# Kernel tuning notes

Measured on AMD Instinct MI355X. Metric: run time of the kernel, lower is better.

Reference implementation:

```python
import jax, jax.numpy as jnp
import numpy as np

BG_ID = 0
RADIUS = 10
MODE = 'gauss'
LAMBDA_B = 1.0
GAMMA = 0.1
TEMP = 4.0
EPS = 1e-8
BIG = 1e6  # stands in for +inf (no fg in a row/column); BIG**2 is fp32-safe


def setup_inputs() -> dict:
    key = jax.random.key(0)
    k1, k2 = jax.random.split(key)
    B, C, H, W = 4, 19, 256, 256
    return {
        'student_logits': jax.random.normal(k1, (B, C, H, W), jnp.float32),
        'teacher_logits': jax.random.normal(k2, (B, C, H, W), jnp.float32),
    }


def _edt2(fg):
    """Exact squared Euclidean distance transform of (1 - fg):
    distance from each pixel to the nearest foreground pixel.
    Separable algorithm: 1D column pass (two cumulative scans), then
    exact lower-envelope minimization along rows (vectorized brute force).
    fg: bool [B, H, W]. Returns float32 [B, H, W]."""
    B, H, W = fg.shape
    ii = jnp.arange(H, dtype=jnp.float32)[None, :, None]  # row index
    # 1D vertical distance to nearest fg pixel in each column
    d_fwd = ii - jax.lax.cummax(jnp.where(fg, ii, -BIG), axis=1)
    d_bwd = -jax.lax.cummax(jnp.where(fg, -ii, -BIG), axis=1, reverse=True) - ii
    g = jnp.minimum(jnp.minimum(d_fwd, d_bwd), BIG)  # [B,H,W]
    # exact 2D squared EDT: dist2[b,i,j] = min_{j'} (j-j')^2 + g[b,i,j']^2
    jj = jnp.arange(W, dtype=jnp.float32)
    diff2 = (jj[:, None] - jj[None, :]) ** 2  # [W, W']
    dist2 = jnp.min(diff2[None, None, :, :] + (g * g)[:, :, None, :], axis=-1)
    return dist2


def _erode(fg):
    """scipy.ndimage.binary_erosion with 4-connected cross structure and
    border_value=0 (out-of-bounds treated as background)."""
    p = jnp.pad(fg, ((0, 0), (1, 1), (1, 1)))
    return fg & p[:, :-2, 1:-1] & p[:, 2:, 1:-1] & p[:, 1:-1, :-2] & p[:, 1:-1, 2:]


def _weight_map(teacher_logits):
    # argmax of softmax(probs) == argmax of logits (softmax is monotone per-pixel)
    pred = jnp.argmax(teacher_logits, axis=1)  # [B,H,W]
    fg = pred != BG_ID
    dist2 = _edt2(fg)
    dist = jnp.sqrt(dist2)
    mask = (dist <= RADIUS).astype(jnp.float32)
    sigma = RADIUS / 2.0
    if MODE == 'gauss':
        wdist = jnp.exp(-dist2 / (2.0 * sigma * sigma))
    else:
        wdist = jnp.clip(1.0 - dist / RADIUS, 0.0, 1.0)
    wdist = wdist * mask
    boundary = (fg & ~_erode(fg)).astype(jnp.float32)
    # wb = wdist*(1+lambda_b*boundary); final weights = wb*mask_inside
    # (if an image has no fg pixels, dist is huge -> mask==0 -> weights==0,
    #  matching the scipy loop's `continue` which leaves zeros)
    return wdist * (1.0 + LAMBDA_B * boundary) * mask


def reference(student_logits, teacher_logits):
    weight_map = _weight_map(teacher_logits)  # [B,H,W]
    # teacher probs at temperature T (torch computes t_prob_T and t_prob
    # identically twice; computed once here)
    t_prob = jax.nn.softmax(teacher_logits / TEMP, axis=1)
    entropy = -jnp.sum(t_prob * jnp.log(jnp.clip(t_prob, EPS, None)), axis=1)
    ent_max = jnp.max(entropy, axis=(1, 2), keepdims=True)
    conf_factor = GAMMA + (1.0 - GAMMA) * (1.0 - entropy / (ent_max + EPS))
    s_logp = jax.nn.log_softmax(student_logits / TEMP, axis=1)
    kl_per_pixel = jnp.sum(t_prob * (jnp.log(t_prob + EPS) - s_logp), axis=1)
    total_weight = weight_map * conf_factor
    loss = jnp.sum(total_weight * kl_per_pixel) / (jnp.sum(total_weight) + EPS)
    return TEMP * TEMP * loss
```

## Files before the change

### kernel.cpp

```cpp
#include <hip/hip_runtime.h>
#include <math.h>

#define NC   19
#define HH   256
#define WW   256
#define NB   4
#define HW   (HH * WW)
#define NPIX (NB * HW)
#define CAP2 121.0f

__global__ __launch_bounds__(256) void k_pixel(
    const float* __restrict__ student, const float* __restrict__ teacher,
    float* __restrict__ entropy, float* __restrict__ kl,
    unsigned char* __restrict__ fg, float* __restrict__ bmax)
{
    const int p = blockIdx.x * 256 + threadIdx.x;
    const int b = p >> 16;
    const int r = p & (HW - 1);
    const float* tb = teacher + (size_t)b * NC * HW + r;
    const float* sb = student + (size_t)b * NC * HW + r;

    float St = 0.f, T1 = 0.f, T2 = 0.f, Ss = 0.f;
    float tmx = -INFINITY;
    int ax = 0;
#pragma unroll
    for (int c = 0; c < NC; ++c) {
        float tv = tb[(size_t)c * HW];
        float sv = sb[(size_t)c * HW];
        if (tv > tmx) { tmx = tv; ax = c; }
        float e = __expf(tv * 0.25f);
        St += e;
        T1 += e * tv;
        T2 += e * sv;
        Ss += __expf(sv * 0.25f);
    }
    float rSt = 1.0f / St;
    float ent = __logf(St) - 0.25f * T1 * rSt;
    float klv = __logf(Ss) - 0.25f * T2 * rSt - ent;

    entropy[p] = ent;
    kl[p]      = klv;
    fg[p]      = (ax != 0) ? 1 : 0;

    float m = ent;
#pragma unroll
    for (int o = 32; o >= 1; o >>= 1) m = fmaxf(m, __shfl_down(m, o, 64));
    __shared__ float red[4];
    int wave = threadIdx.x >> 6, lane = threadIdx.x & 63;
    if (lane == 0) red[wave] = m;
    __syncthreads();
    if (threadIdx.x == 0)
        bmax[blockIdx.x] = fmaxf(fmaxf(red[0], red[1]), fmaxf(red[2], red[3]));
}

#define TS   32
#define HALO 10
#define FW   (TS + 2 * HALO)

__global__ __launch_bounds__(256) void k_tile(
    const unsigned char* __restrict__ fg, const float* __restrict__ entropy,
    const float* __restrict__ kl, const float* __restrict__ bmax,
    double* __restrict__ part)
{
    __shared__ float  fgt[FW][FW];
    __shared__ float  vm[TS][FW];
    __shared__ float  red[4];
    __shared__ double snum[4], sden[4];

    const int b   = blockIdx.z;
    const int ti0 = blockIdx.y * TS;
    const int tj0 = blockIdx.x * TS;
    const int tid = threadIdx.x;
    const int wave = tid >> 6, lane = tid & 63;
    const unsigned char* fgb = fg + (size_t)b * HW;

    float m = bmax[(b << 8) + tid];
#pragma unroll
    for (int o = 32; o >= 1; o >>= 1) m = fmaxf(m, __shfl_down(m, o, 64));
    if (lane == 0) red[wave] = m;

    for (int l = tid; l < FW * FW; l += 256) {
        int li = l / FW, lj = l - li * FW;
        int gi = ti0 - HALO + li, gj = tj0 - HALO + lj;
        float v = 0.f;
        if (gi >= 0 && gi < HH && gj >= 0 && gj < WW) v = (float)fgb[gi * WW + gj];
        fgt[li][lj] = v;
    }
    __syncthreads();
    float em = fmaxf(fmaxf(red[0], red[1]), fmaxf(red[2], red[3]));

    for (int l = tid; l < TS * FW; l += 256) {
        int i = l / FW, jj = l - i * FW;
        float mn = CAP2;
#pragma unroll
        for (int di = -HALO; di <= HALO; ++di) {
            float fv = fgt[HALO + i + di][jj];
            mn = fminf(mn, (float)(di * di) + (1.0f - fv) * 1000.0f);
        }
        vm[i][jj] = mn;
    }
    __syncthreads();

    double num = 0.0, den = 0.0;
#pragma unroll
    for (int k = 0; k < (TS * TS) / 256; ++k) {
        int p = tid + k * 256;
        int i = p >> 5, j = p & (TS - 1);
        float d2 = CAP2;
#pragma unroll
        for (int dj = -HALO; dj <= HALO; ++dj)
            d2 = fminf(d2, (float)(dj * dj) + vm[i][j + HALO + dj]);
        float mask  = (d2 <= 100.0f) ? 1.0f : 0.0f;
        float wdist = __expf(-d2 * 0.02f) * mask;

        float f  = fgt[HALO + i][HALO + j];
        float up = fgt[HALO + i - 1][HALO + j];
        float dn = fgt[HALO + i + 1][HALO + j];
        float lf = fgt[HALO + i][HALO + j - 1];
        float rt = fgt[HALO + i][HALO + j + 1];
        float mn4 = fminf(fminf(up, dn), fminf(lf, rt));
        float boundary = (f != 0.f && mn4 == 0.f) ? 1.0f : 0.0f;

        float w = wdist * (1.0f + boundary) * mask;
        size_t gidx = (size_t)b * HW + (size_t)(ti0 + i) * WW + (tj0 + j);
        float conf = 0.1f + 0.9f * (1.0f - entropy[gidx] / (em + 1e-8f));
        float tw = w * conf;
        num += (double)(tw * kl[gidx]);
        den += (double)tw;
    }

#pragma unroll
    for (int o = 32; o >= 1; o >>= 1) {
        num += __shfl_down(num, o, 64);
        den += __shfl_down(den, o, 64);
    }
    if (lane == 0) { snum[wave] = num; sden[wave] = den; }
    __syncthreads();
    if (tid == 0) {
        int bid = (blockIdx.z << 6) + (blockIdx.y << 3) + blockIdx.x;
        part[bid * 2 + 0] = snum[0] + snum[1] + snum[2] + snum[3];
        part[bid * 2 + 1] = sden[0] + sden[1] + sden[2] + sden[3];
    }
}

__global__ __launch_bounds__(256) void k_final(
    const double* __restrict__ part, float* __restrict__ out)
{
    const int tid = threadIdx.x;
    double num = part[tid * 2 + 0];
    double den = part[tid * 2 + 1];
#pragma unroll
    for (int o = 32; o >= 1; o >>= 1) {
        num += __shfl_down(num, o, 64);
        den += __shfl_down(den, o, 64);
    }
    __shared__ double snum[4], sden[4];
    int wave = tid >> 6, lane = tid & 63;
    if (lane == 0) { snum[wave] = num; sden[wave] = den; }
    __syncthreads();
    if (tid == 0) {
        num = snum[0] + snum[1] + snum[2] + snum[3];
        den = sden[0] + sden[1] + sden[2] + sden[3];
        out[0] = (float)(16.0 * num / (den + 1e-8));
    }
}

extern "C" void kernel_launch(void* const* d_in, const int* in_sizes, int n_in,
                              void* d_out, int out_size, void* d_ws, size_t ws_size,
                              hipStream_t stream)
{
    const float* student = (const float*)d_in[0];
    const float* teacher = (const float*)d_in[1];
    float* out = (float*)d_out;

    char* ws = (char*)d_ws;
    double*        part    = (double*)(ws + 0);
    float*         bmax    = (float*)(ws + 8192);
    float*         entropy = (float*)(ws + 16384);
    float*         kl      = (float*)(ws + 16384 + (size_t)NPIX * 4);
    unsigned char* fg      = (unsigned char*)(ws + 16384 + (size_t)NPIX * 8);

    k_pixel<<<NPIX / 256, 256, 0, stream>>>(student, teacher, entropy, kl, fg, bmax);
    dim3 g2(WW / TS, HH / TS, NB);
    k_tile<<<g2, 256, 0, stream>>>(fg, entropy, kl, bmax, part);
    k_final<<<1, 256, 0, stream>>>(part, out);
}
```

Measured before the change: 87.37 us.

## Vectorize pixel pass and defer confidence normalization to final reduction

The per-pixel kernel now handles two adjacent pixels per thread with float2 loads and writes entropy and KL interleaved as one float2 array. The tile kernel no longer needs the global entropy maximum. It accumulates four weighted sums (w, w*ent, w*kl, w*ent*kl) so the confidence factor, which is linear in entropy, can be applied per batch in the final kernel. This removes the bmax reduction and the second load stream from the tile kernel. The cost is more double-precision accumulators and shuffles, a larger partials buffer, and half as many threads in the pixel kernel.

```diff
diff --git a/kernel.cpp b/kernel.cpp
--- a/kernel.cpp
+++ b/kernel.cpp
@@ -11,38 +11,43 @@
 
 __global__ __launch_bounds__(256) void k_pixel(
     const float* __restrict__ student, const float* __restrict__ teacher,
-    float* __restrict__ entropy, float* __restrict__ kl,
-    unsigned char* __restrict__ fg, float* __restrict__ bmax)
-{
-    const int p = blockIdx.x * 256 + threadIdx.x;
-    const int b = p >> 16;
-    const int r = p & (HW - 1);
+    float2* __restrict__ ekl, unsigned char* __restrict__ fg,
+    float* __restrict__ bmax)
+{
+    const int q = (blockIdx.x * 256 + threadIdx.x) * 2;
+    const int b = q >> 16;
+    const int r = q & (HW - 1);
     const float* tb = teacher + (size_t)b * NC * HW + r;
     const float* sb = student + (size_t)b * NC * HW + r;
 
-    float St = 0.f, T1 = 0.f, T2 = 0.f, Ss = 0.f;
-    float tmx = -INFINITY;
-    int ax = 0;
+    float Stx = 0.f, T1x = 0.f, T2x = 0.f, Ssx = 0.f;
+    float Sty = 0.f, T1y = 0.f, T2y = 0.f, Ssy = 0.f;
+    float tmx = -INFINITY, tmy = -INFINITY;
+    int ax = 0, ay = 0;
 #pragma unroll
     for (int c = 0; c < NC; ++c) {
-        float tv = tb[(size_t)c * HW];
-        float sv = sb[(size_t)c * HW];
-        if (tv > tmx) { tmx = tv; ax = c; }
-        float e = __expf(tv * 0.25f);
-        St += e;
-        T1 += e * tv;
-        T2 += e * sv;
-        Ss += __expf(sv * 0.25f);
-    }
-    float rSt = 1.0f / St;
-    float ent = __logf(St) - 0.25f * T1 * rSt;
-    float klv = __logf(Ss) - 0.25f * T2 * rSt - ent;
-
-    entropy[p] = ent;
-    kl[p]      = klv;
-    fg[p]      = (ax != 0) ? 1 : 0;
-
-    float m = ent;
+        float2 t2 = *(const float2*)(tb + (size_t)c * HW);
+        float2 s2 = *(const float2*)(sb + (size_t)c * HW);
+        if (t2.x > tmx) { tmx = t2.x; ax = c; }
+        if (t2.y > tmy) { tmy = t2.y; ay = c; }
+        float exx = __expf(t2.x * 0.25f);
+        float exy = __expf(t2.y * 0.25f);
+        Stx += exx;           Sty += exy;
+        T1x += exx * t2.x;    T1y += exy * t2.y;
+        T2x += exx * s2.x;    T2y += exy * s2.y;
+        Ssx += __expf(s2.x * 0.25f);
+        Ssy += __expf(s2.y * 0.25f);
+    }
+    float rStx = 1.0f / Stx, rSty = 1.0f / Sty;
+    float entx = __logf(Stx) - 0.25f * T1x * rStx;
+    float enty = __logf(Sty) - 0.25f * T1y * rSty;
+    float klx  = __logf(Ssx) - 0.25f * T2x * rStx - entx;
+    float kly  = __logf(Ssy) - 0.25f * T2y * rSty - enty;
+
+    *(float4*)(ekl + q) = make_float4(entx, klx, enty, kly);
+    *(uchar2*)(fg + q)  = make_uchar2(ax != 0, ay != 0);
+
+    float m = fmaxf(entx, enty);
 #pragma unroll
     for (int o = 32; o >= 1; o >>= 1) m = fmaxf(m, __shfl_down(m, o, 64));
     __shared__ float red[4];
@@ -58,14 +63,12 @@
 #define FW   (TS + 2 * HALO)
 
 __global__ __launch_bounds__(256) void k_tile(
-    const unsigned char* __restrict__ fg, const float* __restrict__ entropy,
-    const float* __restrict__ kl, const float* __restrict__ bmax,
+    const unsigned char* __restrict__ fg, const float2* __restrict__ ekl,
     double* __restrict__ part)
 {
     __shared__ float  fgt[FW][FW];
     __shared__ float  vm[TS][FW];
-    __shared__ float  red[4];
-    __shared__ double snum[4], sden[4];
+    __shared__ double sred[4][4];
 
     const int b   = blockIdx.z;
     const int ti0 = blockIdx.y * TS;
@@ -74,11 +77,6 @@
     const int wave = tid >> 6, lane = tid & 63;
     const unsigned char* fgb = fg + (size_t)b * HW;
 
-    float m = bmax[(b << 8) + tid];
-#pragma unroll
-    for (int o = 32; o >= 1; o >>= 1) m = fmaxf(m, __shfl_down(m, o, 64));
-    if (lane == 0) red[wave] = m;
-
     for (int l = tid; l < FW * FW; l += 256) {
         int li = l / FW, lj = l - li * FW;
         int gi = ti0 - HALO + li, gj = tj0 - HALO + lj;
@@ -87,7 +85,6 @@
         fgt[li][lj] = v;
     }
     __syncthreads();
-    float em = fmaxf(fmaxf(red[0], red[1]), fmaxf(red[2], red[3]));
 
     for (int l = tid; l < TS * FW; l += 256) {
         int i = l / FW, jj = l - i * FW;
@@ -101,7 +98,7 @@
     }
     __syncthreads();
 
-    double num = 0.0, den = 0.0;
+    double s0 = 0.0, s1 = 0.0, s2 = 0.0, s3 = 0.0;
 #pragma unroll
     for (int k = 0; k < (TS * TS) / 256; ++k) {
         int p = tid + k * 256;
@@ -122,45 +119,64 @@
         float boundary = (f != 0.f && mn4 == 0.f) ? 1.0f : 0.0f;
 
         float w = wdist * (1.0f + boundary) * mask;
-        size_t gidx = (size_t)b * HW + (size_t)(ti0 + i) * WW + (tj0 + j);
-        float conf = 0.1f + 0.9f * (1.0f - entropy[gidx] / (em + 1e-8f));
-        float tw = w * conf;
-        num += (double)(tw * kl[gidx]);
-        den += (double)tw;
+        float2 ek = ekl[(size_t)b * HW + (size_t)(ti0 + i) * WW + (tj0 + j)];
+        float we = w * ek.x;
+        s0 += (double)w;
+        s1 += (double)we;
+        s2 += (double)(w * ek.y);
+        s3 += (double)(we * ek.y);
     }
 
 #pragma unroll
     for (int o = 32; o >= 1; o >>= 1) {
-        num += __shfl_down(num, o, 64);
-        den += __shfl_down(den, o, 64);
-    }
-    if (lane == 0) { snum[wave] = num; sden[wave] = den; }
+        s0 += __shfl_down(s0, o, 64);
+        s1 += __shfl_down(s1, o, 64);
+        s2 += __shfl_down(s2, o, 64);
+        s3 += __shfl_down(s3, o, 64);
+    }
+    if (lane == 0) {
+        sred[wave][0] = s0; sred[wave][1] = s1;
+        sred[wave][2] = s2; sred[wave][3] = s3;
+    }
     __syncthreads();
     if (tid == 0) {
         int bid = (blockIdx.z << 6) + (blockIdx.y << 3) + blockIdx.x;
-        part[bid * 2 + 0] = snum[0] + snum[1] + snum[2] + snum[3];
-        part[bid * 2 + 1] = sden[0] + sden[1] + sden[2] + sden[3];
+        double* o = part + bid * 4;
+        o[0] = sred[0][0] + sred[1][0] + sred[2][0] + sred[3][0];
+        o[1] = sred[0][1] + sred[1][1] + sred[2][1] + sred[3][1];
+        o[2] = sred[0][2] + sred[1][2] + sred[2][2] + sred[3][2];
+        o[3] = sred[0][3] + sred[1][3] + sred[2][3] + sred[3][3];
     }
 }
 
 __global__ __launch_bounds__(256) void k_final(
-    const double* __restrict__ part, float* __restrict__ out)
+    const double* __restrict__ part, const float* __restrict__ bmax,
+    float* __restrict__ out)
 {
     const int tid = threadIdx.x;
-    double num = part[tid * 2 + 0];
-    double den = part[tid * 2 + 1];
+    const int b = tid >> 6, lane = tid & 63;
+
+    const double* ps = part + (size_t)(b * 64 + lane) * 4;
+    double s0 = ps[0], s1 = ps[1], s2 = ps[2], s3 = ps[3];
+    float em = fmaxf(bmax[b * 128 + lane], bmax[b * 128 + 64 + lane]);
 #pragma unroll
     for (int o = 32; o >= 1; o >>= 1) {
-        num += __shfl_down(num, o, 64);
-        den += __shfl_down(den, o, 64);
-    }
-    __shared__ double snum[4], sden[4];
-    int wave = tid >> 6, lane = tid & 63;
-    if (lane == 0) { snum[wave] = num; sden[wave] = den; }
+        s0 += __shfl_down(s0, o, 64);
+        s1 += __shfl_down(s1, o, 64);
+        s2 += __shfl_down(s2, o, 64);
+        s3 += __shfl_down(s3, o, 64);
+        em  = fmaxf(em, __shfl_down(em, o, 64));
+    }
+    __shared__ double bnum[4], bden[4];
+    if (lane == 0) {
+        double c = 0.9 / ((double)em + 1e-8);
+        bnum[b] = s2 - c * s3;
+        bden[b] = s0 - c * s1;
+    }
     __syncthreads();
     if (tid == 0) {
-        num = snum[0] + snum[1] + snum[2] + snum[3];
-        den = sden[0] + sden[1] + sden[2] + sden[3];
+        double num = bnum[0] + bnum[1] + bnum[2] + bnum[3];
+        double den = bden[0] + bden[1] + bden[2] + bden[3];
         out[0] = (float)(16.0 * num / (den + 1e-8));
     }
 }
@@ -174,14 +190,13 @@
     float* out = (float*)d_out;
 
     char* ws = (char*)d_ws;
-    double*        part    = (double*)(ws + 0);
-    float*         bmax    = (float*)(ws + 8192);
-    float*         entropy = (float*)(ws + 16384);
-    float*         kl      = (float*)(ws + 16384 + (size_t)NPIX * 4);
-    unsigned char* fg      = (unsigned char*)(ws + 16384 + (size_t)NPIX * 8);
-
-    k_pixel<<<NPIX / 256, 256, 0, stream>>>(student, teacher, entropy, kl, fg, bmax);
+    double*        part = (double*)(ws + 0);
+    float*         bmax = (float*)(ws + 16384);
+    float2*        ekl  = (float2*)(ws + 32768);
+    unsigned char* fg   = (unsigned char*)(ws + 32768 + (size_t)NPIX * 8);
+
+    k_pixel<<<NPIX / 2 / 256, 256, 0, stream>>>(student, teacher, ekl, fg, bmax);
     dim3 g2(WW / TS, HH / TS, NB);
-    k_tile<<<g2, 256, 0, stream>>>(fg, entropy, kl, bmax, part);
-    k_final<<<1, 256, 0, stream>>>(part, out);
-}
+    k_tile<<<g2, 256, 0, stream>>>(fg, ekl, part);
+    k_final<<<1, 256, 0, stream>>>(part, bmax, out);
+}
```

Result: no change. 88.15 us (+0.9%).
